# Optimization experiments

Hardware: AMD Instinct MI355X
Metric: run time of the kernel (lower is better)

Reference implementation:

```python
import jax, jax.numpy as jnp
import numpy as np

B, L = 64, 1024
ENC_DIM, DEC_DIM, ATT_DIM = 512, 512, 512


def setup_inputs() -> dict:
    key = jax.random.key(0)
    ks = jax.random.split(key, 11)
    s_enc = 1.0 / np.sqrt(ENC_DIM)
    s_dec = 1.0 / np.sqrt(DEC_DIM)
    s_att = 1.0 / np.sqrt(ATT_DIM)
    return {
        "encoder_features": jax.random.normal(ks[0], (B, L, ENC_DIM), jnp.float32),
        "decoder_hidden": jax.random.normal(ks[1], (B, DEC_DIM), jnp.float32),
        "coverage": jax.random.uniform(ks[2], (B, L), jnp.float32),
        # nn.Linear params (torch stores weight as [out, in]; we keep [in, out])
        "W_enc": jax.random.uniform(ks[3], (ENC_DIM, ATT_DIM), jnp.float32, -s_enc, s_enc),
        "b_enc": jax.random.uniform(ks[4], (ATT_DIM,), jnp.float32, -s_enc, s_enc),
        "W_dec": jax.random.uniform(ks[5], (DEC_DIM, ATT_DIM), jnp.float32, -s_dec, s_dec),
        "b_dec": jax.random.uniform(ks[6], (ATT_DIM,), jnp.float32, -s_dec, s_dec),
        "W_cov": jax.random.uniform(ks[7], (1, ATT_DIM), jnp.float32, -1.0, 1.0),
        "b_cov": jax.random.uniform(ks[8], (ATT_DIM,), jnp.float32, -1.0, 1.0),
        "W_full": jax.random.uniform(ks[9], (ATT_DIM, 1), jnp.float32, -s_att, s_att),
        "b_full": jax.random.uniform(ks[10], (1,), jnp.float32, -s_att, s_att),
    }


def reference(encoder_features, decoder_hidden, coverage,
              W_enc, b_enc, W_dec, b_dec, W_cov, b_cov, W_full, b_full):
    # att1: [B, L, A]
    att1 = jnp.einsum("ble,ea->bla", encoder_features, W_enc) + b_enc
    # att2: [B, 1, A]
    att2 = (decoder_hidden @ W_dec + b_dec)[:, None, :]
    # att3: coverage[B,L] through Linear(1, A) -> outer product, [B, L, A]
    att3 = coverage[:, :, None] * W_cov[0] + b_cov
    # energy: [B, L]
    energy = (jax.nn.relu(att1 + att2 + att3) @ W_full)[:, :, 0] + b_full[0]
    alpha = jax.nn.softmax(energy, axis=1)  # [B, L]
    new_coverage = coverage + alpha
    attention_weighted_encoding = jnp.einsum("ble,bl->be", encoder_features, alpha)
    return (attention_weighted_encoding, alpha, new_coverage)
```

## Files before the change

### kernel.cpp

```cpp
#include <hip/hip_runtime.h>
#include <cstdint>
#include <cstddef>

#define NB   64
#define NL   1024
#define NA   512
#define NE   512

typedef __attribute__((ext_vector_type(8))) short bf16x8;
typedef __attribute__((ext_vector_type(4))) float f32x4;

__device__ __forceinline__ unsigned short f2bf(float x){
    unsigned int u = __float_as_uint(x);
    u += 0x7FFFu + ((u >> 16) & 1u);
    return (unsigned short)(u >> 16);
}

__global__ __launch_bounds__(256) void k_wfrag(const float* __restrict__ Wenc,
                                               unsigned short* __restrict__ wfrag){
    const int g    = blockIdx.x * 256 + threadIdx.x;
    const int lane = g & 63;
    const int n    = (g >> 6) & 3;
    const int ks   = (g >> 8) & 1;
    const int cw   = (g >> 9) & 7;
    const int s    = g >> 12;
    const int col  = cw * 64 + n * 16 + (lane & 15);
    const int kb   = s * 64 + ks * 32 + (lane >> 4) * 8;
    unsigned int w[4];
    #pragma unroll
    for (int p = 0; p < 4; ++p){
        unsigned short lo = f2bf(Wenc[(size_t)(kb + 2*p    ) * NA + col]);
        unsigned short hi = f2bf(Wenc[(size_t)(kb + 2*p + 1) * NA + col]);
        w[p] = (unsigned int)lo | ((unsigned int)hi << 16);
    }
    ((uint4*)wfrag)[g] = make_uint4(w[0], w[1], w[2], w[3]);
}

__global__ __launch_bounds__(256) void k_base(const float* __restrict__ dh,
                                              const float* __restrict__ Wdec,
                                              const float* __restrict__ bdec,
                                              const float* __restrict__ benc,
                                              const float* __restrict__ bcov,
                                              float* __restrict__ base){
    const int b   = blockIdx.x >> 3;
    const int a0  = (blockIdx.x & 7) * 64;
    const int tid = threadIdx.x;
    const int al  = tid & 63, kg = tid >> 6;
    __shared__ float h[512];
    __shared__ float ps[4][64];
    h[tid]       = dh[b * 512 + tid];
    h[tid + 256] = dh[b * 512 + tid + 256];
    __syncthreads();
    const float* wp = Wdec + (size_t)(kg * 128) * 512 + a0 + al;
    const float* hp = h + kg * 128;
    float s0 = 0.f, s1 = 0.f, s2 = 0.f, s3 = 0.f;
    #pragma unroll
    for (int k = 0; k < 128; k += 4){
        s0 += hp[k + 0] * wp[(size_t)(k + 0) * 512];
        s1 += hp[k + 1] * wp[(size_t)(k + 1) * 512];
        s2 += hp[k + 2] * wp[(size_t)(k + 2) * 512];
        s3 += hp[k + 3] * wp[(size_t)(k + 3) * 512];
    }
    ps[kg][al] = (s0 + s1) + (s2 + s3);
    __syncthreads();
    if (tid < 64){
        const int a = a0 + tid;
        base[b * 512 + a] = ps[0][tid] + ps[1][tid] + ps[2][tid] + ps[3][tid]
                          + bdec[a] + benc[a] + bcov[a];
    }
}

__global__ __launch_bounds__(512, 2) void k_energy(
        const float* __restrict__ enc,
        const float* __restrict__ cov,
        const float* __restrict__ base,
        const unsigned short* __restrict__ wfrag,
        const float* __restrict__ Wcov,
        const float* __restrict__ Wfull,
        float* __restrict__ energy)
{
    __shared__ __align__(16) unsigned char sA[2][16384];
    __shared__ float sEp[8][128];
    __shared__ float sCov[128];

    const int tid  = threadIdx.x;
    const int wid  = tid >> 6, lane = tid & 63;
    const int r0   = blockIdx.x * 128;
    const int b    = r0 >> 10;

    if (tid < 128) sCov[tid] = cov[r0 + tid];

    const int rloc = tid >> 2, q = tid & 3;
    const float* arow = enc + (size_t)(r0 + rloc) * NE + q * 16;
    const int awoff = ((q >> 1) * 8 + (rloc >> 4)) * 1024
                    + ((rloc & 15) + 32 * (q & 1)) * 16;

    const bf16x8* bbase = (const bf16x8*)wfrag + wid * 512 + lane;

    f32x4 acc[8][4];
    #pragma unroll
    for (int m = 0; m < 8; ++m)
        #pragma unroll
        for (int n = 0; n < 4; ++n) acc[m][n] = (f32x4){0.f, 0.f, 0.f, 0.f};

    bf16x8 bc0[4], bc1[4];
    #pragma unroll
    for (int j = 0; j < 4; ++j) bc0[j] = bbase[j * 64];
    #pragma unroll
    for (int j = 0; j < 4; ++j) bc1[j] = bbase[256 + j * 64];
    {
        float4 v0 = *(const float4*)(arow);
        float4 v1 = *(const float4*)(arow + 4);
        float4 v2 = *(const float4*)(arow + 8);
        float4 v3 = *(const float4*)(arow + 12);
        uint4 f1, f2;
        f1.x = f2bf(v0.x) | ((unsigned)f2bf(v0.y) << 16);
        f1.y = f2bf(v0.z) | ((unsigned)f2bf(v0.w) << 16);
        f1.z = f2bf(v1.x) | ((unsigned)f2bf(v1.y) << 16);
        f1.w = f2bf(v1.z) | ((unsigned)f2bf(v1.w) << 16);
        f2.x = f2bf(v2.x) | ((unsigned)f2bf(v2.y) << 16);
        f2.y = f2bf(v2.z) | ((unsigned)f2bf(v2.w) << 16);
        f2.z = f2bf(v3.x) | ((unsigned)f2bf(v3.y) << 16);
        f2.w = f2bf(v3.z) | ((unsigned)f2bf(v3.w) << 16);
        *(uint4*)(sA[0] + awoff)       = f1;
        *(uint4*)(sA[0] + awoff + 256) = f2;
    }
    __syncthreads();

    #pragma unroll
    for (int s = 0; s < 8; ++s){
        const int cb = s & 1;
        float4 av0, av1, av2, av3;
        if (s < 7){
            const float* ap = arow + (s + 1) * 64;
            av0 = *(const float4*)(ap);
            av1 = *(const float4*)(ap + 4);
            av2 = *(const float4*)(ap + 8);
            av3 = *(const float4*)(ap + 12);
        }
        {
            bf16x8 af[8];
            #pragma unroll
            for (int m = 0; m < 8; ++m)
                af[m] = *(const bf16x8*)(sA[cb] + m * 1024 + lane * 16);
            #pragma unroll
            for (int n = 0; n < 4; ++n)
                #pragma unroll
                for (int m = 0; m < 8; ++m)
                    acc[m][n] = __builtin_amdgcn_mfma_f32_16x16x32_bf16(
                                    af[m], bc0[n], acc[m][n], 0, 0, 0);
        }
        if (s < 7){
            const bf16x8* bp = bbase + (s + 1) * 4096;
            #pragma unroll
            for (int j = 0; j < 4; ++j) bc0[j] = bp[j * 64];
        }
        {
            bf16x8 af[8];
            #pragma unroll
            for (int m = 0; m < 8; ++m)
                af[m] = *(const bf16x8*)(sA[cb] + (8 + m) * 1024 + lane * 16);
            #pragma unroll
            for (int n = 0; n < 4; ++n)
                #pragma unroll
                for (int m = 0; m < 8; ++m)
                    acc[m][n] = __builtin_amdgcn_mfma_f32_16x16x32_bf16(
                                    af[m], bc1[n], acc[m][n], 0, 0, 0);
        }
        if (s < 7){
            const bf16x8* bp = bbase + (s + 1) * 4096 + 256;
            #pragma unroll
            for (int j = 0; j < 4; ++j) bc1[j] = bp[j * 64];
            uint4 f1, f2;
            f1.x = f2bf(av0.x) | ((unsigned)f2bf(av0.y) << 16);
            f1.y = f2bf(av0.z) | ((unsigned)f2bf(av0.w) << 16);
            f1.z = f2bf(av1.x) | ((unsigned)f2bf(av1.y) << 16);
            f1.w = f2bf(av1.z) | ((unsigned)f2bf(av1.w) << 16);
            f2.x = f2bf(av2.x) | ((unsigned)f2bf(av2.y) << 16);
            f2.y = f2bf(av2.z) | ((unsigned)f2bf(av2.w) << 16);
            f2.z = f2bf(av3.x) | ((unsigned)f2bf(av3.y) << 16);
            f2.w = f2bf(av3.z) | ((unsigned)f2bf(av3.w) << 16);
            *(uint4*)(sA[cb ^ 1] + awoff)       = f1;
            *(uint4*)(sA[cb ^ 1] + awoff + 256) = f2;
        }
        __syncthreads();
    }

    const int c0 = wid * 64 + (lane & 15);
    float basev[4], wcovv[4], wfullv[4];
    #pragma unroll
    for (int n = 0; n < 4; ++n){
        const int c = c0 + n * 16;
        basev[n]  = base[b * 512 + c];
        wcovv[n]  = Wcov[c];
        wfullv[n] = Wfull[c];
    }
    const int hi = lane >> 4;
    float epv[8][4];
    #pragma unroll
    for (int m = 0; m < 8; ++m){
        #pragma unroll
        for (int r = 0; r < 4; ++r){
            const float cv = sCov[m * 16 + 4 * hi + r];
            float e = 0.f;
            #pragma unroll
            for (int n = 0; n < 4; ++n){
                float v = acc[m][n][r] + basev[n] + cv * wcovv[n];
                v = fmaxf(v, 0.f);
                e += v * wfullv[n];
            }
            epv[m][r] = e;
        }
    }
    #pragma unroll
    for (int m = 0; m < 8; ++m)
        #pragma unroll
        for (int r = 0; r < 4; ++r){
            float v = epv[m][r];
            v += __shfl_xor(v, 1);
            v += __shfl_xor(v, 2);
            v += __shfl_xor(v, 4);
            v += __shfl_xor(v, 8);
            epv[m][r] = v;
        }
    if ((lane & 15) == 0){
        #pragma unroll
        for (int m = 0; m < 8; ++m)
            #pragma unroll
            for (int r = 0; r < 4; ++r)
                sEp[wid][m * 16 + 4 * hi + r] = epv[m][r];
    }
    __syncthreads();
    if (tid < 128)
        energy[r0 + tid] = ((sEp[0][tid] + sEp[1][tid]) + (sEp[2][tid] + sEp[3][tid]))
                         + ((sEp[4][tid] + sEp[5][tid]) + (sEp[6][tid] + sEp[7][tid]));
}

#define AWE_OFF   0
#define ALPHA_OFF 32768
#define NCOV_OFF  98304

__global__ __launch_bounds__(256) void k_finish(
        const float* __restrict__ enc, const float* __restrict__ cov,
        const float* __restrict__ energy, float* __restrict__ out)
{
    const int bid = blockIdx.x;
    const int b = bid >> 3, ec = bid & 7;
    const int tid = threadIdx.x;
    __shared__ float sa[1024];
    __shared__ float rb[16];
    __shared__ float ps2[16][64];

    float4 ev = ((const float4*)(energy + b * 1024))[tid];
    float mx = fmaxf(fmaxf(ev.x, ev.y), fmaxf(ev.z, ev.w));
    #pragma unroll
    for (int off = 32; off; off >>= 1) mx = fmaxf(mx, __shfl_xor(mx, off));
    if ((tid & 63) == 0) rb[tid >> 6] = mx;
    __syncthreads();
    mx = fmaxf(fmaxf(rb[0], rb[1]), fmaxf(rb[2], rb[3]));
    float e0 = __expf(ev.x - mx), e1 = __expf(ev.y - mx),
          e2 = __expf(ev.z - mx), e3 = __expf(ev.w - mx);
    ((float4*)sa)[tid] = make_float4(e0, e1, e2, e3);
    float sm = e0 + e1 + e2 + e3;
    #pragma unroll
    for (int off = 32; off; off >>= 1) sm += __shfl_xor(sm, off);
    if ((tid & 63) == 0) rb[8 + (tid >> 6)] = sm;
    __syncthreads();
    const float inv = 1.0f / (rb[8] + rb[9] + rb[10] + rb[11]);

    if (ec == 0){
        #pragma unroll
        for (int i = 0; i < 4; ++i){
            const int idx = tid + i * 256;
            const float a = sa[idx] * inv;
            out[ALPHA_OFF + b * 1024 + idx] = a;
            out[NCOV_OFF  + b * 1024 + idx] = cov[b * 1024 + idx] + a;
        }
    }

    const int cg = tid & 15, rg = tid >> 4;
    const float4* ep = (const float4*)(enc + (size_t)(b * 1024 + rg * 64) * 512)
                     + ec * 16 + cg;
    const float* w = sa + rg * 64;
    float ax = 0.f, ay = 0.f, az = 0.f, aw = 0.f;
    #pragma unroll 8
    for (int l = 0; l < 64; ++l){
        float4 e4 = ep[(size_t)l * 128];
        const float wl = w[l];
        ax += e4.x * wl; ay += e4.y * wl; az += e4.z * wl; aw += e4.w * wl;
    }
    ps2[rg][cg * 4 + 0] = ax;
    ps2[rg][cg * 4 + 1] = ay;
    ps2[rg][cg * 4 + 2] = az;
    ps2[rg][cg * 4 + 3] = aw;
    __syncthreads();
    if (tid < 64){
        float s = 0.f;
        #pragma unroll
        for (int g = 0; g < 16; ++g) s += ps2[g][tid];
        out[AWE_OFF + b * 512 + ec * 64 + tid] = s * inv;
    }
}

extern "C" void kernel_launch(void* const* d_in, const int* in_sizes, int n_in,
                              void* d_out, int out_size, void* d_ws, size_t ws_size,
                              hipStream_t stream){
    const float* enc   = (const float*)d_in[0];
    const float* dh    = (const float*)d_in[1];
    const float* cov   = (const float*)d_in[2];
    const float* Wenc  = (const float*)d_in[3];
    const float* benc  = (const float*)d_in[4];
    const float* Wdec  = (const float*)d_in[5];
    const float* bdec  = (const float*)d_in[6];
    const float* Wcov  = (const float*)d_in[7];
    const float* bcov  = (const float*)d_in[8];
    const float* Wfull = (const float*)d_in[9];
    float* out = (float*)d_out;

    unsigned short* wfrag = (unsigned short*)d_ws;
    float* base   = (float*)((char*)d_ws + 512 * 1024);
    float* energy = (float*)((char*)d_ws + 640 * 1024);

    k_wfrag <<<128,  256, 0, stream>>>(Wenc, wfrag);
    k_base  <<<512,  256, 0, stream>>>(dh, Wdec, bdec, benc, bcov, base);
    k_energy<<<512,  512, 0, stream>>>(enc, cov, base, wfrag, Wcov, Wfull, energy);
    k_finish<<<512,  256, 0, stream>>>(enc, cov, energy, out);
}
```

Before: 78.54 us.

## Merge prep kernels and split energy GEMM columns across blocks with atomics

Fuses the W_enc fragment packing, the decoder base projection and an energy zero-fill into one prep launch, removing a kernel launch. The energy kernel now uses 64-row tiles with the 512 attention columns split across two 256-thread blocks, giving 2048 blocks instead of 512 for better CU occupancy. Partial energies are combined with float atomicAdd into a pre-zeroed buffer. The cost is that each encoder row tile is loaded and converted to bf16 twice, and the atomic summation order is nondeterministic.

```diff
diff --git a/kernel.cpp b/kernel.cpp
--- a/kernel.cpp
+++ b/kernel.cpp
@@ -16,61 +16,67 @@
     return (unsigned short)(u >> 16);
 }
 
-__global__ __launch_bounds__(256) void k_wfrag(const float* __restrict__ Wenc,
-                                               unsigned short* __restrict__ wfrag){
-    const int g    = blockIdx.x * 256 + threadIdx.x;
-    const int lane = g & 63;
-    const int n    = (g >> 6) & 3;
-    const int ks   = (g >> 8) & 1;
-    const int cw   = (g >> 9) & 7;
-    const int s    = g >> 12;
-    const int col  = cw * 64 + n * 16 + (lane & 15);
-    const int kb   = s * 64 + ks * 32 + (lane >> 4) * 8;
-    unsigned int w[4];
-    #pragma unroll
-    for (int p = 0; p < 4; ++p){
-        unsigned short lo = f2bf(Wenc[(size_t)(kb + 2*p    ) * NA + col]);
-        unsigned short hi = f2bf(Wenc[(size_t)(kb + 2*p + 1) * NA + col]);
-        w[p] = (unsigned int)lo | ((unsigned int)hi << 16);
-    }
-    ((uint4*)wfrag)[g] = make_uint4(w[0], w[1], w[2], w[3]);
-}
-
-__global__ __launch_bounds__(256) void k_base(const float* __restrict__ dh,
+__global__ __launch_bounds__(256) void k_prep(const float* __restrict__ Wenc,
+                                              unsigned short* __restrict__ wfrag,
+                                              const float* __restrict__ dh,
                                               const float* __restrict__ Wdec,
                                               const float* __restrict__ bdec,
                                               const float* __restrict__ benc,
                                               const float* __restrict__ bcov,
-                                              float* __restrict__ base){
-    const int b   = blockIdx.x >> 3;
-    const int a0  = (blockIdx.x & 7) * 64;
-    const int tid = threadIdx.x;
-    const int al  = tid & 63, kg = tid >> 6;
-    __shared__ float h[512];
-    __shared__ float ps[4][64];
-    h[tid]       = dh[b * 512 + tid];
-    h[tid + 256] = dh[b * 512 + tid + 256];
-    __syncthreads();
-    const float* wp = Wdec + (size_t)(kg * 128) * 512 + a0 + al;
-    const float* hp = h + kg * 128;
-    float s0 = 0.f, s1 = 0.f, s2 = 0.f, s3 = 0.f;
-    #pragma unroll
-    for (int k = 0; k < 128; k += 4){
-        s0 += hp[k + 0] * wp[(size_t)(k + 0) * 512];
-        s1 += hp[k + 1] * wp[(size_t)(k + 1) * 512];
-        s2 += hp[k + 2] * wp[(size_t)(k + 2) * 512];
-        s3 += hp[k + 3] * wp[(size_t)(k + 3) * 512];
-    }
-    ps[kg][al] = (s0 + s1) + (s2 + s3);
-    __syncthreads();
-    if (tid < 64){
-        const int a = a0 + tid;
-        base[b * 512 + a] = ps[0][tid] + ps[1][tid] + ps[2][tid] + ps[3][tid]
-                          + bdec[a] + benc[a] + bcov[a];
-    }
-}
-
-__global__ __launch_bounds__(512, 2) void k_energy(
+                                              float* __restrict__ base,
+                                              float* __restrict__ energy){
+    const int bid = blockIdx.x, tid = threadIdx.x;
+    if (bid < 128){
+        const int g    = bid * 256 + tid;
+        const int lane = g & 63;
+        const int n    = (g >> 6) & 3;
+        const int ks   = (g >> 8) & 1;
+        const int cw   = (g >> 9) & 7;
+        const int s    = g >> 12;
+        const int col  = cw * 64 + n * 16 + (lane & 15);
+        const int kb   = s * 64 + ks * 32 + (lane >> 4) * 8;
+        unsigned int w[4];
+        #pragma unroll
+        for (int p = 0; p < 4; ++p){
+            unsigned short lo = f2bf(Wenc[(size_t)(kb + 2*p    ) * NA + col]);
+            unsigned short hi = f2bf(Wenc[(size_t)(kb + 2*p + 1) * NA + col]);
+            w[p] = (unsigned int)lo | ((unsigned int)hi << 16);
+        }
+        ((uint4*)wfrag)[g] = make_uint4(w[0], w[1], w[2], w[3]);
+    } else if (bid < 640){
+        const int idx = bid - 128;
+        const int b   = idx >> 3;
+        const int a0  = (idx & 7) * 64;
+        const int al  = tid & 63, kg = tid >> 6;
+        __shared__ float h[512];
+        __shared__ float ps[4][64];
+        h[tid]       = dh[b * 512 + tid];
+        h[tid + 256] = dh[b * 512 + tid + 256];
+        __syncthreads();
+        const float* wp = Wdec + (size_t)(kg * 128) * 512 + a0 + al;
+        const float* hp = h + kg * 128;
+        float s0 = 0.f, s1 = 0.f, s2 = 0.f, s3 = 0.f;
+        #pragma unroll
+        for (int k = 0; k < 128; k += 4){
+            s0 += hp[k + 0] * wp[(size_t)(k + 0) * 512];
+            s1 += hp[k + 1] * wp[(size_t)(k + 1) * 512];
+            s2 += hp[k + 2] * wp[(size_t)(k + 2) * 512];
+            s3 += hp[k + 3] * wp[(size_t)(k + 3) * 512];
+        }
+        ps[kg][al] = (s0 + s1) + (s2 + s3);
+        __syncthreads();
+        if (tid < 64){
+            const int a = a0 + tid;
+            base[b * 512 + a] = ps[0][tid] + ps[1][tid] + ps[2][tid] + ps[3][tid]
+                              + bdec[a] + benc[a] + bcov[a];
+        }
+    } else {
+        const int idx = bid - 640;
+        ((float4*)energy)[idx * 256 + tid] = make_float4(0.f, 0.f, 0.f, 0.f);
+    }
+}
+
+__global__ __launch_bounds__(256, 2) void k_energy(
         const float* __restrict__ enc,
         const float* __restrict__ cov,
         const float* __restrict__ base,
@@ -79,27 +85,30 @@
         const float* __restrict__ Wfull,
         float* __restrict__ energy)
 {
-    __shared__ __align__(16) unsigned char sA[2][16384];
-    __shared__ float sEp[8][128];
-    __shared__ float sCov[128];
+    __shared__ __align__(16) unsigned char sA[2][8192];
+    __shared__ float sEp[4][64];
+    __shared__ float sCov[64];
 
     const int tid  = threadIdx.x;
     const int wid  = tid >> 6, lane = tid & 63;
-    const int r0   = blockIdx.x * 128;
-    const int b    = r0 >> 10;
-
-    if (tid < 128) sCov[tid] = cov[r0 + tid];
+    const int rt   = blockIdx.x >> 1;
+    const int ch   = blockIdx.x & 1;
+    const int r0   = rt * 64;
+    const int b    = rt >> 4;
+    const int cwav = ch * 4 + wid;
+
+    if (tid < 64) sCov[tid] = cov[r0 + tid];
 
     const int rloc = tid >> 2, q = tid & 3;
     const float* arow = enc + (size_t)(r0 + rloc) * NE + q * 16;
-    const int awoff = ((q >> 1) * 8 + (rloc >> 4)) * 1024
+    const int awoff = ((q >> 1) * 4 + (rloc >> 4)) * 1024
                     + ((rloc & 15) + 32 * (q & 1)) * 16;
 
-    const bf16x8* bbase = (const bf16x8*)wfrag + wid * 512 + lane;
-
-    f32x4 acc[8][4];
-    #pragma unroll
-    for (int m = 0; m < 8; ++m)
+    const bf16x8* bbase = (const bf16x8*)wfrag + cwav * 512 + lane;
+
+    f32x4 acc[4][4];
+    #pragma unroll
+    for (int m = 0; m < 4; ++m)
         #pragma unroll
         for (int n = 0; n < 4; ++n) acc[m][n] = (f32x4){0.f, 0.f, 0.f, 0.f};
 
@@ -139,14 +148,14 @@
             av3 = *(const float4*)(ap + 12);
         }
         {
-            bf16x8 af[8];
-            #pragma unroll
-            for (int m = 0; m < 8; ++m)
+            bf16x8 af[4];
+            #pragma unroll
+            for (int m = 0; m < 4; ++m)
                 af[m] = *(const bf16x8*)(sA[cb] + m * 1024 + lane * 16);
             #pragma unroll
             for (int n = 0; n < 4; ++n)
                 #pragma unroll
-                for (int m = 0; m < 8; ++m)
+                for (int m = 0; m < 4; ++m)
                     acc[m][n] = __builtin_amdgcn_mfma_f32_16x16x32_bf16(
                                     af[m], bc0[n], acc[m][n], 0, 0, 0);
         }
@@ -156,14 +165,14 @@
             for (int j = 0; j < 4; ++j) bc0[j] = bp[j * 64];
         }
         {
-            bf16x8 af[8];
-            #pragma unroll
-            for (int m = 0; m < 8; ++m)
-                af[m] = *(const bf16x8*)(sA[cb] + (8 + m) * 1024 + lane * 16);
+            bf16x8 af[4];
+            #pragma unroll
+            for (int m = 0; m < 4; ++m)
+                af[m] = *(const bf16x8*)(sA[cb] + (4 + m) * 1024 + lane * 16);
             #pragma unroll
             for (int n = 0; n < 4; ++n)
                 #pragma unroll
-                for (int m = 0; m < 8; ++m)
+                for (int m = 0; m < 4; ++m)
                     acc[m][n] = __builtin_amdgcn_mfma_f32_16x16x32_bf16(
                                     af[m], bc1[n], acc[m][n], 0, 0, 0);
         }
@@ -186,7 +195,7 @@
         __syncthreads();
     }
 
-    const int c0 = wid * 64 + (lane & 15);
+    const int c0 = cwav * 64 + (lane & 15);
     float basev[4], wcovv[4], wfullv[4];
     #pragma unroll
     for (int n = 0; n < 4; ++n){
@@ -196,9 +205,9 @@
         wfullv[n] = Wfull[c];
     }
     const int hi = lane >> 4;
-    float epv[8][4];
-    #pragma unroll
-    for (int m = 0; m < 8; ++m){
+    float epv[4][4];
+    #pragma unroll
+    for (int m = 0; m < 4; ++m){
         #pragma unroll
         for (int r = 0; r < 4; ++r){
             const float cv = sCov[m * 16 + 4 * hi + r];
@@ -213,7 +222,7 @@
         }
     }
     #pragma unroll
-    for (int m = 0; m < 8; ++m)
+    for (int m = 0; m < 4; ++m)
         #pragma unroll
         for (int r = 0; r < 4; ++r){
             float v = epv[m][r];
@@ -225,15 +234,16 @@
         }
     if ((lane & 15) == 0){
         #pragma unroll
-        for (int m = 0; m < 8; ++m)
+        for (int m = 0; m < 4; ++m)
             #pragma unroll
             for (int r = 0; r < 4; ++r)
                 sEp[wid][m * 16 + 4 * hi + r] = epv[m][r];
     }
     __syncthreads();
-    if (tid < 128)
-        energy[r0 + tid] = ((sEp[0][tid] + sEp[1][tid]) + (sEp[2][tid] + sEp[3][tid]))
-                         + ((sEp[4][tid] + sEp[5][tid]) + (sEp[6][tid] + sEp[7][tid]));
+    if (tid < 64){
+        const float part = (sEp[0][tid] + sEp[1][tid]) + (sEp[2][tid] + sEp[3][tid]);
+        atomicAdd(energy + r0 + tid, part);
+    }
 }
 
 #define AWE_OFF   0
@@ -321,8 +331,8 @@
     float* base   = (float*)((char*)d_ws + 512 * 1024);
     float* energy = (float*)((char*)d_ws + 640 * 1024);
 
-    k_wfrag <<<128,  256, 0, stream>>>(Wenc, wfrag);
-    k_base  <<<512,  256, 0, stream>>>(dh, Wdec, bdec, benc, bcov, base);
-    k_energy<<<512,  512, 0, stream>>>(enc, cov, base, wfrag, Wcov, Wfull, energy);
+    k_prep  <<<704,  256, 0, stream>>>(Wenc, wfrag, dh, Wdec, bdec, benc, bcov,
+                                       base, energy);
+    k_energy<<<2048, 256, 0, stream>>>(enc, cov, base, wfrag, Wcov, Wfull, energy);
     k_finish<<<512,  256, 0, stream>>>(enc, cov, energy, out);
 }
```

Measured after the change: 97.66 us. 1.24x slower.
